# Kernel optimization log

Measured on AMD Instinct MI355X. Metric: run time of the kernel, lower is better.

The kernel has to match this reference:

```python
import jax, jax.numpy as jnp
import numpy as np

B = 512          # batch
IN_UNITS = 8     # primary capsule dim
IN_CH = 1152     # number of primary capsules
NUM_UNITS = 10   # output capsules (classes)
UNIT_SIZE = 16   # output capsule dim
BETA = 1.45      # squash beta: 1.45 - 0.22*(ep_iter/total) with ep_iter = n_iter = 0
NUM_ROUTING = 3


def setup_inputs() -> dict:
    key = jax.random.key(0)
    k1, k2 = jax.random.split(key)
    x = jax.random.normal(k1, (B, IN_UNITS, IN_CH), dtype=jnp.float32)
    # W parameter: torch shape (1, in_channels, num_units, unit_size, in_units); drop leading 1
    W = jax.random.normal(k2, (IN_CH, NUM_UNITS, UNIT_SIZE, IN_UNITS), dtype=jnp.float32)
    return {"x": x, "W": W}


def _squash(s):
    # s: (B, num_units, unit_size). Torch squash sums dim=2 of (B,1,nu,us,1),
    # which is the num_units axis (axis=1 here). Faithful to source.
    mag_sq = jnp.sum(s * s, axis=1, keepdims=True)          # (B,1,us)
    mag = jnp.sqrt(mag_sq)
    return mag_sq / (BETA + mag_sq) * (s / mag)


def reference(x, W):
    # u_hat[b,i,j,u] = sum_k W[i,j,u,k] * x[b,k,i]
    u_hat = jnp.einsum('ijuk,bki->biju', W, x)               # (B, IN_CH, NUM_UNITS, UNIT_SIZE)
    b_ij = jnp.zeros((IN_CH, NUM_UNITS), dtype=x.dtype)
    v = None
    for _ in range(NUM_ROUTING):
        c = jax.nn.softmax(b_ij, axis=0)                     # softmax over in_channels (dim=1 in torch)
        s = jnp.einsum('ij,biju->bju', c, u_hat)             # (B, NUM_UNITS, UNIT_SIZE)
        v = _squash(s)
        # b update: agreement <u_hat, v>, averaged over batch
        b_ij = jnp.einsum('biju,bju->ij', u_hat, v) / u_hat.shape[0]
    # rearrange 'b c (g h) w -> b c g (h w)' with g=4, w=1 -> reshape (B, nu, 4, us//4)
    return v.reshape(v.shape[0], NUM_UNITS, 4, UNIT_SIZE // 4)
```

## Files before the change

### kernel.cpp

```cpp
#include <hip/hip_runtime.h>
#include <hip/hip_bf16.h>
#include <math.h>

#define B    512
#define INU  8
#define IC   1152
#define NU   10
#define US   16
#define JU   160
#define KI   9216
#define BETAC 1.45f
#define NSPLIT 32
#define KC 288

typedef __attribute__((ext_vector_type(8))) __bf16 bf16x8;
typedef __attribute__((ext_vector_type(4))) float floatx4;

static __device__ __forceinline__ unsigned short f2bf(float f) {
  unsigned u = __builtin_bit_cast(unsigned, f);
  u = (u + 0x7fffu + ((u >> 16) & 1u)) >> 16;
  return (unsigned short)u;
}
static __device__ __forceinline__ float bf2f(unsigned short h) {
  return __builtin_bit_cast(float, ((unsigned)h) << 16);
}
static __device__ __forceinline__ uint4 scale8(uint4 wv, float4 cA, float4 cB) {
  union { uint4 u; unsigned short s[8]; } in;
  in.u = wv;
  union { uint4 u; __hip_bfloat162 h[4]; } o;
  o.h[0] = __float22bfloat162_rn(make_float2(bf2f(in.s[0]) * cA.x, bf2f(in.s[1]) * cA.y));
  o.h[1] = __float22bfloat162_rn(make_float2(bf2f(in.s[2]) * cA.z, bf2f(in.s[3]) * cA.w));
  o.h[2] = __float22bfloat162_rn(make_float2(bf2f(in.s[4]) * cB.x, bf2f(in.s[5]) * cB.y));
  o.h[3] = __float22bfloat162_rn(make_float2(bf2f(in.s[6]) * cB.z, bf2f(in.s[7]) * cB.w));
  return o.u;
}

__global__ __launch_bounds__(256) void prep_kernel(
    const float* __restrict__ x, const float* __restrict__ W,
    unsigned short* __restrict__ xb, unsigned short* __restrict__ xT,
    unsigned short* __restrict__ Wt, float* __restrict__ Wr,
    float* __restrict__ cT) {
  __shared__ float ts[32 * 322];
  int id = blockIdx.x;
  int t = threadIdx.x;
  if (id < 1152) {
    int k0 = (id % 144) * 64;
    int b0 = (id / 144) * 64;
#pragma unroll
    for (int r = 0; r < 16; ++r) {
      int idx = t + 256 * r;
      int br = idx >> 6, kc = idx & 63;
      float v = x[(size_t)(b0 + br) * KI + k0 + kc];
      ts[br * 65 + kc] = v;
      xb[(size_t)(b0 + br) * KI + k0 + kc] = f2bf(v);
    }
    __syncthreads();
#pragma unroll
    for (int r = 0; r < 8; ++r) {
      int idx = t + 256 * r;
      int kr = idx >> 5, bc = (idx & 31) * 2;
      unsigned lo = f2bf(ts[bc * 65 + kr]);
      unsigned hi = f2bf(ts[(bc + 1) * 65 + kr]);
      *(unsigned*)&xT[(size_t)(k0 + kr) * B + b0 + bc] = lo | (hi << 16);
    }
  } else {
    int wid = id - 1152;
    int i0 = (wid >> 2) * 32;
    int c0 = (wid & 3) * 320;
#pragma unroll
    for (int r = 0; r < 20; ++r) {
      int q = t + 256 * r;
      int il = q / 160, c = (q - il * 160) * 2;
      *(float2*)&ts[il * 322 + c] =
          *(const float2*)&W[(size_t)(i0 + il) * 1280 + c0 + c];
    }
    __syncthreads();
    {
      int il2 = (t & 15) * 2;
      for (int p = (t >> 4); p < 320; p += 16) {
        int c = c0 + p;
        int ju = c >> 3, k = c & 7;
        unsigned lo = f2bf(ts[il2 * 322 + p]);
        unsigned hi = f2bf(ts[(il2 + 1) * 322 + p]);
        *(unsigned*)&Wt[(size_t)ju * KI + k * IC + i0 + il2] = lo | (hi << 16);
      }
    }
    int ju0 = c0 >> 3;
    for (int q = t; q < 8 * 32 * 40; q += 256) {
      int k = q / 1280;
      int il = (q / 40) & 31;
      int jl = q - (q / 40) * 40;
      Wr[((size_t)k * IC + i0 + il) * JU + ju0 + jl] = ts[il * 322 + jl * 8 + k];
    }
    if (id == 1152) {
      for (int q = t; q < IC * NU; q += 256) cT[q] = 1.0f / (float)IC;
    }
  }
}

__global__ __launch_bounds__(256) void s_gemm_mfma(
    const unsigned short* __restrict__ xb, const unsigned short* __restrict__ Wt,
    const float* __restrict__ cT, float* __restrict__ sp) {
  int b0 = blockIdx.x * 64;
  int kbase = blockIdx.y * KC;
  int i0 = kbase % IC;
  int t = threadIdx.x;
  int w = t >> 6, lane = t & 63, col = lane & 15, quad = lane >> 4;
  __shared__ unsigned short xs[64 * 40];
  __shared__ unsigned short ms[160 * 40];
  __shared__ float cs[NU * KC];

  int xrow = t >> 2, xc = (t & 3) * 8;
  int mrow0 = t >> 2, mrow1 = (t + 256) >> 2, mrow2 = (t + 512) >> 2;
  int mc = (t & 3) * 8;
  int j0 = mrow0 >> 4, j1 = mrow1 >> 4, j2 = mrow2 >> 4;

  for (int ch = t; ch < NU * KC; ch += 256) {
    int j = ch / KC;
    cs[ch] = cT[j * IC + i0 + (ch - j * KC)];
  }
  uint4 xv, m0, m1, m2;
  auto prefetch = [&](int k0) {
    xv = *(const uint4*)&xb[(size_t)(b0 + xrow) * KI + k0 + xc];
    m0 = *(const uint4*)&Wt[(size_t)mrow0 * KI + k0 + mc];
    m1 = *(const uint4*)&Wt[(size_t)mrow1 * KI + k0 + mc];
    if (t < 128) m2 = *(const uint4*)&Wt[(size_t)mrow2 * KI + k0 + mc];
  };
  auto commit = [&](int off) {
    *(uint4*)&xs[xrow * 40 + xc] = xv;
    float4 a0 = *(const float4*)&cs[j0 * KC + off + mc];
    float4 a1 = *(const float4*)&cs[j0 * KC + off + mc + 4];
    *(uint4*)&ms[mrow0 * 40 + mc] = scale8(m0, a0, a1);
    float4 b0c = *(const float4*)&cs[j1 * KC + off + mc];
    float4 b1c = *(const float4*)&cs[j1 * KC + off + mc + 4];
    *(uint4*)&ms[mrow1 * 40 + mc] = scale8(m1, b0c, b1c);
    if (t < 128) {
      float4 d0 = *(const float4*)&cs[j2 * KC + off + mc];
      float4 d1 = *(const float4*)&cs[j2 * KC + off + mc + 4];
      *(uint4*)&ms[mrow2 * 40 + mc] = scale8(m2, d0, d1);
    }
  };
  floatx4 acc[10];
#pragma unroll
  for (int jt = 0; jt < 10; ++jt) acc[jt] = (floatx4){0.f, 0.f, 0.f, 0.f};
  prefetch(kbase);
  __syncthreads();
  const int nsteps = KC >> 5;
  for (int s = 0; s < nsteps; ++s) {
    commit(s * 32);
    __syncthreads();
    if (s + 1 < nsteps) prefetch(kbase + (s + 1) * 32);
    bf16x8 a = *(bf16x8*)&xs[(w * 16 + col) * 40 + quad * 8];
#pragma unroll
    for (int jt = 0; jt < 10; ++jt) {
      bf16x8 bb = *(bf16x8*)&ms[(jt * 16 + col) * 40 + quad * 8];
      acc[jt] = __builtin_amdgcn_mfma_f32_16x16x32_bf16(a, bb, acc[jt], 0, 0, 0);
    }
    __syncthreads();
  }
#pragma unroll
  for (int jt = 0; jt < 10; ++jt)
#pragma unroll
    for (int r = 0; r < 4; ++r) {
      int b = b0 + w * 16 + quad * 4 + r;
      sp[((size_t)blockIdx.y * B + b) * JU + jt * 16 + col] = acc[jt][r];
    }
}

__global__ __launch_bounds__(192) void squash_kernel(
    const float* __restrict__ sp, unsigned short* __restrict__ vT,
    float* __restrict__ out) {
  int b = blockIdx.x;
  int t = threadIdx.x;
  __shared__ float sv[JU];
  __shared__ float fac[US];
  float s = 0.0f;
  if (t < JU) {
#pragma unroll
    for (int k = 0; k < NSPLIT; ++k) s += sp[((size_t)k * B + b) * JU + t];
    sv[t] = s;
  }
  __syncthreads();
  if (t < US) {
    float m = 0.0f;
#pragma unroll
    for (int j = 0; j < NU; ++j) {
      float q = sv[j * US + t];
      m += q * q;
    }
    fac[t] = sqrtf(m) / (BETAC + m);
  }
  __syncthreads();
  if (t < JU) {
    float val = s * fac[t & 15];
    vT[(size_t)t * B + b] = f2bf(val);
    if (out) out[(size_t)b * JU + t] = val;
  }
}

__global__ __launch_bounds__(256) void b_update_mfma(
    const unsigned short* __restrict__ xT, const unsigned short* __restrict__ vT,
    const float* __restrict__ Wr, float* __restrict__ bp) {
  int k = blockIdx.x / 18;
  int i0 = (blockIdx.x - k * 18) * 64;
  int bs = blockIdx.y;
  size_t ki0 = (size_t)k * IC + i0;
  int t = threadIdx.x;
  int w = t >> 6, lane = t & 63, col = lane & 15, quad = lane >> 4;
  __shared__ unsigned short xs[64 * 40];
  __shared__ unsigned short vs[160 * 40];
  int xrow = t >> 2, xc = (t & 3) * 8;
  int mrow0 = t >> 2, mrow1 = (t + 256) >> 2, mrow2 = (t + 512) >> 2;
  int mc = (t & 3) * 8;
  uint4 xv, m0, m1, m2;
  auto prefetch = [&](int c0) {
    xv = *(const uint4*)&xT[(ki0 + xrow) * B + c0 + xc];
    m0 = *(const uint4*)&vT[(size_t)mrow0 * B + c0 + mc];
    m1 = *(const uint4*)&vT[(size_t)mrow1 * B + c0 + mc];
    if (t < 128) m2 = *(const uint4*)&vT[(size_t)mrow2 * B + c0 + mc];
  };
  auto commit = [&]() {
    *(uint4*)&xs[xrow * 40 + xc] = xv;
    *(uint4*)&vs[mrow0 * 40 + mc] = m0;
    *(uint4*)&vs[mrow1 * 40 + mc] = m1;
    if (t < 128) *(uint4*)&vs[mrow2 * 40 + mc] = m2;
  };
  floatx4 acc[10];
#pragma unroll
  for (int jt = 0; jt < 10; ++jt) acc[jt] = (floatx4){0.f, 0.f, 0.f, 0.f};
  prefetch(bs * 256);
  for (int s = 0; s < 8; ++s) {
    commit();
    __syncthreads();
    if (s < 7) prefetch(bs * 256 + (s + 1) * 32);
    bf16x8 a = *(bf16x8*)&xs[(w * 16 + col) * 40 + quad * 8];
#pragma unroll
    for (int jt = 0; jt < 10; ++jt) {
      bf16x8 bb = *(bf16x8*)&vs[(jt * 16 + col) * 40 + quad * 8];
      acc[jt] = __builtin_amdgcn_mfma_f32_16x16x32_bf16(a, bb, acc[jt], 0, 0, 0);
    }
    __syncthreads();
  }
  int p = k * 2 + bs;
#pragma unroll
  for (int jt = 0; jt < 10; ++jt) {
#pragma unroll
    for (int r = 0; r < 4; ++r) {
      int i = i0 + w * 16 + quad * 4 + r;
      float wv = Wr[((size_t)k * IC + i) * JU + jt * 16 + col];
      float pr = wv * acc[jt][r];
      pr += __shfl_xor(pr, 1);
      pr += __shfl_xor(pr, 2);
      pr += __shfl_xor(pr, 4);
      pr += __shfl_xor(pr, 8);
      if (col == 0)
        bp[(size_t)p * (IC * NU) + jt * IC + i] = pr * (1.0f / (float)B);
    }
  }
}

__global__ __launch_bounds__(256) void softmax_c_kernel(
    const float* __restrict__ bp, float* __restrict__ cT) {
  int j = blockIdx.x;
  int t = threadIdx.x;
  __shared__ float bsum[IC];
  __shared__ float red[256];
  for (int i = t; i < IC; i += 256) {
    float s = 0.0f;
#pragma unroll
    for (int p = 0; p < 16; ++p) s += bp[(size_t)p * (IC * NU) + j * IC + i];
    bsum[i] = s;
  }
  __syncthreads();
  float m = -1e30f;
  for (int i = t; i < IC; i += 256) m = fmaxf(m, bsum[i]);
  red[t] = m;
  __syncthreads();
  for (int o = 128; o > 0; o >>= 1) {
    if (t < o) red[t] = fmaxf(red[t], red[t + o]);
    __syncthreads();
  }
  float mx = red[0];
  __syncthreads();
  float sm = 0.0f;
  for (int i = t; i < IC; i += 256) {
    float e = __expf(bsum[i] - mx);
    bsum[i] = e;
    sm += e;
  }
  red[t] = sm;
  __syncthreads();
  for (int o = 128; o > 0; o >>= 1) {
    if (t < o) red[t] += red[t + o];
    __syncthreads();
  }
  float inv = 1.0f / red[0];
  for (int i = t; i < IC; i += 256) cT[(size_t)j * IC + i] = bsum[i] * inv;
}

extern "C" void kernel_launch(void* const* d_in, const int* in_sizes, int n_in,
                              void* d_out, int out_size, void* d_ws,
                              size_t ws_size, hipStream_t stream) {
  const float* x = (const float*)d_in[0];
  const float* W = (const float*)d_in[1];
  float* out = (float*)d_out;

  char* pws = (char*)d_ws;
  float* cT = (float*)pws;                     pws += (size_t)NU * IC * 4;
  float* bp = (float*)pws;                     pws += (size_t)16 * IC * NU * 4;
  float* sp = (float*)pws;                     pws += (size_t)NSPLIT * B * JU * 4;
  float* Wr = (float*)pws;                     pws += (size_t)KI * JU * 4;
  unsigned short* xb = (unsigned short*)pws;   pws += (size_t)B * KI * 2;
  unsigned short* xT = (unsigned short*)pws;   pws += (size_t)KI * B * 2;
  unsigned short* Wt = (unsigned short*)pws;   pws += (size_t)JU * KI * 2;
  unsigned short* vT = (unsigned short*)pws;

  prep_kernel<<<1152 + 144, 256, 0, stream>>>(x, W, xb, xT, Wt, Wr, cT);

  for (int it = 0; it < 3; ++it) {
    s_gemm_mfma<<<dim3(8, NSPLIT), 256, 0, stream>>>(xb, Wt, cT, sp);
    squash_kernel<<<B, 192, 0, stream>>>(sp, vT, (it == 2) ? out : nullptr);
    if (it < 2) {
      b_update_mfma<<<dim3(144, 2), 256, 0, stream>>>(xT, vT, Wr, bp);
      softmax_c_kernel<<<NU, 256, 0, stream>>>(bp, cT);
    }
  }
}
```

Measured before the change: 176.9 us.

## Fuse softmax into b_update via atomic accumulation and last-block ticket

Replaces the per-partition b partial buffer with atomic adds into a single b_ij array, zeroed by the squash kernel. The last b_update block, found with an atomic ticket counter, computes the softmax over in-channels for all output units and writes c. This removes the separate softmax launch and the 16-way partial reduction. In exchange, one block now runs the softmax serially and the atomics make the summation order nondeterministic.

```diff
diff --git a/kernel.cpp b/kernel.cpp
--- a/kernel.cpp
+++ b/kernel.cpp
@@ -169,9 +169,14 @@
 
 __global__ __launch_bounds__(192) void squash_kernel(
     const float* __restrict__ sp, unsigned short* __restrict__ vT,
-    float* __restrict__ out) {
+    float* __restrict__ out, float* __restrict__ bij,
+    unsigned* __restrict__ ticket) {
   int b = blockIdx.x;
   int t = threadIdx.x;
+  if (b == 0) {
+    for (int q = t; q < IC * NU; q += 192) bij[q] = 0.0f;
+    if (t == 0) ticket[0] = 0u;
+  }
   __shared__ float sv[JU];
   __shared__ float fac[US];
   float s = 0.0f;
@@ -200,7 +205,8 @@
 
 __global__ __launch_bounds__(256) void b_update_mfma(
     const unsigned short* __restrict__ xT, const unsigned short* __restrict__ vT,
-    const float* __restrict__ Wr, float* __restrict__ bp) {
+    const float* __restrict__ Wr, float* __restrict__ bij,
+    float* __restrict__ cT, unsigned* __restrict__ ticket) {
   int k = blockIdx.x / 18;
   int i0 = (blockIdx.x - k * 18) * 64;
   int bs = blockIdx.y;
@@ -209,6 +215,7 @@
   int w = t >> 6, lane = t & 63, col = lane & 15, quad = lane >> 4;
   __shared__ unsigned short xs[64 * 40];
   __shared__ unsigned short vs[160 * 40];
+  __shared__ int sflag;
   int xrow = t >> 2, xc = (t & 3) * 8;
   int mrow0 = t >> 2, mrow1 = (t + 256) >> 2, mrow2 = (t + 512) >> 2;
   int mc = (t & 3) * 8;
@@ -241,7 +248,6 @@
     }
     __syncthreads();
   }
-  int p = k * 2 + bs;
 #pragma unroll
   for (int jt = 0; jt < 10; ++jt) {
 #pragma unroll
@@ -254,48 +260,50 @@
       pr += __shfl_xor(pr, 4);
       pr += __shfl_xor(pr, 8);
       if (col == 0)
-        bp[(size_t)p * (IC * NU) + jt * IC + i] = pr * (1.0f / (float)B);
-    }
-  }
-}
-
-__global__ __launch_bounds__(256) void softmax_c_kernel(
-    const float* __restrict__ bp, float* __restrict__ cT) {
-  int j = blockIdx.x;
-  int t = threadIdx.x;
-  __shared__ float bsum[IC];
-  __shared__ float red[256];
-  for (int i = t; i < IC; i += 256) {
-    float s = 0.0f;
-#pragma unroll
-    for (int p = 0; p < 16; ++p) s += bp[(size_t)p * (IC * NU) + j * IC + i];
-    bsum[i] = s;
-  }
-  __syncthreads();
-  float m = -1e30f;
-  for (int i = t; i < IC; i += 256) m = fmaxf(m, bsum[i]);
-  red[t] = m;
-  __syncthreads();
-  for (int o = 128; o > 0; o >>= 1) {
-    if (t < o) red[t] = fmaxf(red[t], red[t + o]);
-    __syncthreads();
-  }
-  float mx = red[0];
-  __syncthreads();
-  float sm = 0.0f;
-  for (int i = t; i < IC; i += 256) {
-    float e = __expf(bsum[i] - mx);
-    bsum[i] = e;
-    sm += e;
-  }
-  red[t] = sm;
-  __syncthreads();
-  for (int o = 128; o > 0; o >>= 1) {
-    if (t < o) red[t] += red[t + o];
-    __syncthreads();
-  }
-  float inv = 1.0f / red[0];
-  for (int i = t; i < IC; i += 256) cT[(size_t)j * IC + i] = bsum[i] * inv;
+        atomicAdd(&bij[jt * IC + i], pr * (1.0f / (float)B));
+    }
+  }
+  __syncthreads();
+  if (t == 0) {
+    __threadfence();
+    sflag = (atomicAdd(ticket, 1u) == 287u) ? 1 : 0;
+  }
+  __syncthreads();
+  if (sflag) {
+    __threadfence();
+    float* fb = (float*)xs;
+    float* red = (float*)vs;
+    for (int j = 0; j < NU; ++j) {
+      for (int i = t; i < IC; i += 256) fb[i] = bij[j * IC + i];
+      __syncthreads();
+      float ml = -1e30f;
+      for (int i = t; i < IC; i += 256) ml = fmaxf(ml, fb[i]);
+      red[t] = ml;
+      __syncthreads();
+      for (int o = 128; o > 0; o >>= 1) {
+        if (t < o) red[t] = fmaxf(red[t], red[t + o]);
+        __syncthreads();
+      }
+      float mx = red[0];
+      __syncthreads();
+      float sl = 0.0f;
+      for (int i = t; i < IC; i += 256) {
+        float e = __expf(fb[i] - mx);
+        fb[i] = e;
+        sl += e;
+      }
+      red[t] = sl;
+      __syncthreads();
+      for (int o = 128; o > 0; o >>= 1) {
+        if (t < o) red[t] += red[t + o];
+        __syncthreads();
+      }
+      float inv = 1.0f / red[0];
+      __syncthreads();
+      for (int i = t; i < IC; i += 256) cT[j * IC + i] = fb[i] * inv;
+      __syncthreads();
+    }
+  }
 }
 
 extern "C" void kernel_launch(void* const* d_in, const int* in_sizes, int n_in,
@@ -307,7 +315,8 @@
 
   char* pws = (char*)d_ws;
   float* cT = (float*)pws;                     pws += (size_t)NU * IC * 4;
-  float* bp = (float*)pws;                     pws += (size_t)16 * IC * NU * 4;
+  float* bij = (float*)pws;                    pws += (size_t)NU * IC * 4;
+  unsigned* ticket = (unsigned*)pws;           pws += 256;
   float* sp = (float*)pws;                     pws += (size_t)NSPLIT * B * JU * 4;
   float* Wr = (float*)pws;                     pws += (size_t)KI * JU * 4;
   unsigned short* xb = (unsigned short*)pws;   pws += (size_t)B * KI * 2;
@@ -319,10 +328,11 @@
 
   for (int it = 0; it < 3; ++it) {
     s_gemm_mfma<<<dim3(8, NSPLIT), 256, 0, stream>>>(xb, Wt, cT, sp);
-    squash_kernel<<<B, 192, 0, stream>>>(sp, vT, (it == 2) ? out : nullptr);
+    squash_kernel<<<B, 192, 0, stream>>>(sp, vT, (it == 2) ? out : nullptr,
+                                         bij, ticket);
     if (it < 2) {
-      b_update_mfma<<<dim3(144, 2), 256, 0, stream>>>(xT, vT, Wr, bp);
-      softmax_c_kernel<<<NU, 256, 0, stream>>>(bp, cT);
-    }
-  }
-}
+      b_update_mfma<<<dim3(144, 2), 256, 0, stream>>>(xT, vT, Wr, bij, cT,
+                                                      ticket);
+    }
+  }
+}
```

Result: slower. 248.9 us (+40.6%).
